# Kernel tuning notes

Hardware: AMD Instinct MI355X
Metric: run time of the kernel (lower is better)

The kernel has to match this reference:

```python
import jax, jax.numpy as jnp
import numpy as np
from itertools import product

N = 300000          # active voxels
CIN, C = 16, 32     # input / conv channels
K = 27              # 3x3x3 kernel volume
Z, Y, X = 41, 1024, 1024  # sparse spatial shape (grid_size[::-1] + [1,0,0])
B = 2               # batch size
EPS = 1e-3          # BatchNorm eps (matches norm_fn eps=0.001)


def _build_coords_and_rulebook(rng):
    # unique active coords per batch element
    total = Z * Y * X
    per = N // B
    coords = []
    for b in range(B):
        lin = np.unique(rng.integers(0, total, size=int(per * 1.3)))
        rng.shuffle(lin)
        lin = lin[:per]
        assert lin.shape[0] == per
        z = lin // (Y * X)
        y = (lin % (Y * X)) // X
        x = lin % X
        coords.append(np.stack([np.full(per, b), z, y, x], axis=1))
    coords = np.concatenate(coords, axis=0).astype(np.int64)  # [N,4]

    # hash-free rulebook via sorted linear keys + searchsorted
    key = ((coords[:, 0] * Z + coords[:, 1]) * Y + coords[:, 2]) * X + coords[:, 3]
    perm = np.argsort(key)
    skey = key[perm]
    nbr = np.full((N, K), -1, dtype=np.int32)
    bz, zz, yy, xx = coords[:, 0], coords[:, 1], coords[:, 2], coords[:, 3]
    for k, (dz, dy, dx) in enumerate(product((-1, 0, 1), repeat=3)):
        nz, ny, nx = zz + dz, yy + dy, xx + dx
        valid = (nz >= 0) & (nz < Z) & (ny >= 0) & (ny < Y) & (nx >= 0) & (nx < X)
        nkey = ((bz * Z + nz) * Y + ny) * X + nx
        pos = np.searchsorted(skey, nkey)
        pos = np.clip(pos, 0, N - 1)
        found = valid & (skey[pos] == nkey)
        nbr[:, k] = np.where(found, perm[pos], -1).astype(np.int32)
    return coords, nbr


def _bn_params(k, c):
    k1, k2, k3, k4 = jax.random.split(k, 4)
    gamma = jax.random.uniform(k1, (c,), minval=0.5, maxval=1.5)
    beta = jax.random.normal(k2, (c,)) * 0.1
    mean = jax.random.normal(k3, (c,)) * 0.1
    var = jax.random.uniform(k4, (c,), minval=0.5, maxval=1.5)
    return jnp.stack([gamma, beta, mean, var], axis=0)  # [4,C]


def setup_inputs() -> dict:
    rng = np.random.default_rng(0)
    _, nbr = _build_coords_and_rulebook(rng)

    key = jax.random.key(0)
    ks = jax.random.split(key, 12)
    feat = jax.random.normal(ks[0], (N, CIN), dtype=jnp.float32)

    def conv_w(k, cin, cout):
        return jax.random.normal(k, (K, cin, cout), dtype=jnp.float32) * (1.0 / np.sqrt(K * cin))

    return {
        "voxel_features": feat,
        "neighbor_idx": jnp.asarray(nbr),
        "w_in": conv_w(ks[1], CIN, C), "bn_in": _bn_params(ks[2], C),
        "w1a": conv_w(ks[3], C, C), "bn1a": _bn_params(ks[4], C),
        "w1b": conv_w(ks[5], C, C), "bn1b": _bn_params(ks[6], C),
        "w2a": conv_w(ks[7], C, C), "bn2a": _bn_params(ks[8], C),
        "w2b": conv_w(ks[9], C, C), "bn2b": _bn_params(ks[10], C),
    }


def reference(voxel_features, neighbor_idx, w_in, bn_in, w1a, bn1a, w1b, bn1b,
              w2a, bn2a, w2b, bn2b):
    def bn(x, p):
        gamma, beta, mean, var = p
        return gamma * (x - mean) * jax.lax.rsqrt(var + EPS) + beta

    def subm(feat, w):
        # submanifold conv: gather active neighbors, GEMM per kernel offset, accumulate
        out = jnp.zeros((feat.shape[0], w.shape[2]), feat.dtype)
        for k in range(K):
            idx = neighbor_idx[:, k]
            g = jnp.where((idx >= 0)[:, None], feat[jnp.maximum(idx, 0)], 0.0)
            out = out + g @ w[k]
        return out

    # conv_input: SubMConv3d + BN + ReLU
    x = jax.nn.relu(bn(subm(voxel_features, w_in), bn_in))
    # conv1: two SparseBasicBlocks (conv-bn-relu-conv-bn + residual, relu)
    for wa, bna, wb, bnb in ((w1a, bn1a, w1b, bn1b), (w2a, bn2a, w2b, bn2b)):
        identity = x
        x = jax.nn.relu(bn(subm(x, wa), bna))
        x = bn(subm(x, wb), bnb)
        x = jax.nn.relu(x + identity)
    # voxel importance (vis_importance branch, minus file IO / sorting side effects)
    voxel_importance = jax.nn.sigmoid(jnp.mean(jnp.abs(x), axis=1, keepdims=True))
    return x, voxel_importance
```

## Files before the change

### kernel.cpp

```cpp
#include <hip/hip_runtime.h>
#include <hip/hip_bf16.h>
#include <hip/hip_fp16.h>
#include <cstdint>
#include <cstddef>

#define NVOX 300000
#define KNBR 27
#define COUT 32
#define CINP 32
#define NT   (NVOX / 16)
#define RB   ((NVOX + 255) / 256)
#define WFIXE (5 * KNBR * CINP * COUT)
#define WFB  ((WFIXE + 255) / 256)
#define WDE  (5 * COUT * CINP)
#define WDB  ((WDE + 255) / 256)

typedef __hip_bfloat16 bf16;
typedef _Float16 half8 __attribute__((ext_vector_type(8)));
typedef float floatx4 __attribute__((ext_vector_type(4)));
typedef unsigned short ushort8 __attribute__((ext_vector_type(8)));

__device__ __forceinline__ float bf2f(unsigned short u) {
    union { unsigned int i; float f; } x; x.i = ((unsigned int)u) << 16; return x.f;
}
__device__ __forceinline__ int detect_fp32(const void* b0) {
    const unsigned short* p = (const unsigned short*)b0;
    int hits = 0;
    for (int i = 0; i < 16; i++) {
        float v = bf2f(p[2 * i]);
        if (v >= 0.25f && v <= 4.0f) hits++;
    }
    return (hits >= 8) ? 0 : 1;
}
__device__ __forceinline__ float rdw(const void* w, int rel, int fp32) {
    return fp32 ? ((const float*)w)[rel] : __bfloat162float(((const bf16*)w)[rel]);
}


__global__ __launch_bounds__(256)
void setup_kernel(const int* __restrict__ nbr,
                  const void* w0, const void* w1, const void* w2, const void* w3, const void* w4,
                  const void* b0, const void* b1, const void* b2, const void* b3, const void* b4,
                  float* __restrict__ wfix, __half* __restrict__ wtf,
                  float* __restrict__ bnab,
                  int* __restrict__ flag, int* __restrict__ counter,
                  int* __restrict__ cvlist) {
    const int tid = threadIdx.x;

    if (blockIdx.x < RB) {
        __shared__ int flags[256];
        __shared__ int wsum[4];
        __shared__ int wbase[4];
        flags[tid] = 0;
        __syncthreads();
        const int base = blockIdx.x * 256;
        const int nvox = (NVOX - base < 256) ? (NVOX - base) : 256;
        const int nI4  = (nvox * KNBR) >> 2;
        const int4* p4 = (const int4*)(nbr + (size_t)base * KNBR);
        for (int i = tid; i < nI4; i += 256) {
            const int4 q = p4[i];
            if ((q.x & q.y & q.z & q.w) < 0) continue;
            const unsigned t = (unsigned)(i << 2);
            if (q.x >= 0) { unsigned u = t;     unsigned lv = (u * 4855u) >> 17; if (u - lv * 27u != 13u) flags[lv] = 1; }
            if (q.y >= 0) { unsigned u = t + 1; unsigned lv = (u * 4855u) >> 17; if (u - lv * 27u != 13u) flags[lv] = 1; }
            if (q.z >= 0) { unsigned u = t + 2; unsigned lv = (u * 4855u) >> 17; if (u - lv * 27u != 13u) flags[lv] = 1; }
            if (q.w >= 0) { unsigned u = t + 3; unsigned lv = (u * 4855u) >> 17; if (u - lv * 27u != 13u) flags[lv] = 1; }
        }
        __syncthreads();
        const int v = base + tid;
        const bool f = (tid < nvox) && (flags[tid] != 0);
        const unsigned long long wm = __ballot(f);
        const int wd = tid >> 6, ln = tid & 63;
        if (ln == 0) wsum[wd] = __popcll(wm);
        __syncthreads();
        if (tid == 0) {
            int t0 = wsum[0], t1 = wsum[1], t2 = wsum[2], t3 = wsum[3];
            int tot = t0 + t1 + t2 + t3;
            int b = tot ? atomicAdd(counter, tot) : 0;
            wbase[0] = b; wbase[1] = b + t0; wbase[2] = b + t0 + t1; wbase[3] = b + t0 + t1 + t2;
        }
        __syncthreads();
        if (f) cvlist[wbase[wd] + __popcll(wm & ((1ULL << ln) - 1ULL))] = v;
        return;
    }

    const int fp32 = detect_fp32(b0);

    if (blockIdx.x < RB + WFB) {
        int i = (blockIdx.x - RB) * 256 + tid;
        if (i >= WFIXE) return;
        int L   = i / (KNBR * CINP * COUT);
        int rem = i % (KNBR * CINP * COUT);
        int k   = rem / (CINP * COUT);
        int kk  = (rem / COUT) % CINP;
        int nn  = rem % COUT;
        const void* w = (L == 0) ? w0 : (L == 1) ? w1 : (L == 2) ? w2 : (L == 3) ? w3 : w4;
        int cinL = (L == 0) ? 16 : 32;
        wfix[i] = (kk < cinL) ? rdw(w, (k * cinL + kk) * COUT + nn, fp32) : 0.f;
        return;
    }

    if (blockIdx.x < RB + WFB + WDB) {
        int i = (blockIdx.x - RB - WFB) * 256 + tid;
        if (i >= WDE) return;
        int L  = i / (COUT * CINP);
        int nn = (i / CINP) % COUT;
        int kk = i % CINP;
        const void* w = (L == 0) ? w0 : (L == 1) ? w1 : (L == 2) ? w2 : (L == 3) ? w3 : w4;
        int cinL = (L == 0) ? 16 : 32;
        int sk = (L == 0) ? kk : ((kk & 1) ? 16 + (kk >> 1) : (kk >> 1));
        float val = (sk < cinL) ? rdw(w, (13 * cinL + sk) * COUT + nn, fp32) : 0.f;
        wtf[i] = __float2half(val);
        return;
    }

    if (tid == 192) *flag = fp32;
    if (tid < 160) {
        int L = tid / 32, c = tid % 32;
        const void* b = (L == 0) ? b0 : (L == 1) ? b1 : (L == 2) ? b2 : (L == 3) ? b3 : b4;
        float g, be, m, v;
        if (fp32) {
            const float* q = (const float*)b;
            g = q[c]; be = q[32 + c]; m = q[64 + c]; v = q[96 + c];
        } else {
            const bf16* q = (const bf16*)b;
            g = __bfloat162float(q[c]); be = __bfloat162float(q[32 + c]);
            m = __bfloat162float(q[64 + c]); v = __bfloat162float(q[96 + c]);
        }
        float a = g * rsqrtf(v + 1e-3f);
        bnab[L * 64 + c]      = a;
        bnab[L * 64 + 32 + c] = be - a * m;
    }
}

__global__ __launch_bounds__(256)
void dense_fused(const void* __restrict__ feat,
                 const __half* __restrict__ wtf,
                 const float* __restrict__ bnab,
                 void* __restrict__ out_base,
                 const int* __restrict__ flag) {
    __shared__ __align__(16) _Float16 ldsT[4][16][40];
    const int gw   = (blockIdx.x * 256 + threadIdx.x) >> 6;
    const int nw   = (gridDim.x * 256) >> 6;
    const int wv   = threadIdx.x >> 6;
    const int lane = threadIdx.x & 63;
    const int n    = lane & 15;
    const int quad = lane >> 4;
    const int fp32 = *flag;

    half8 bfa[5], bfb[5];
    float a0[5], b0v[5], a1[5], b1v[5];
#pragma unroll
    for (int L = 0; L < 5; L++) {
        bfa[L] = *(const half8*)((const _Float16*)wtf + L * 1024 + n * 32 + quad * 8);
        bfb[L] = *(const half8*)((const _Float16*)wtf + L * 1024 + (n + 16) * 32 + quad * 8);
        a0[L] = bnab[L * 64 + n];      b0v[L] = bnab[L * 64 + 32 + n];
        a1[L] = bnab[L * 64 + 16 + n]; b1v[L] = bnab[L * 64 + 48 + n];
    }

    for (int t = gw; t < NT; t += nw) {
        const int v0 = t * 16;
        half8 af = {};
        if (quad < 2) {
            if (fp32) {
                const float* p = (const float*)feat + (size_t)(v0 + n) * 16 + quad * 8;
                const float4 u0 = *(const float4*)p;
                const float4 u1 = *(const float4*)(p + 4);
                af[0] = (_Float16)u0.x; af[1] = (_Float16)u0.y; af[2] = (_Float16)u0.z; af[3] = (_Float16)u0.w;
                af[4] = (_Float16)u1.x; af[5] = (_Float16)u1.y; af[6] = (_Float16)u1.z; af[7] = (_Float16)u1.w;
            } else {
                const ushort8 u = *(const ushort8*)((const unsigned short*)feat + (size_t)(v0 + n) * 16 + quad * 8);
#pragma unroll
                for (int j = 0; j < 8; j++) af[j] = (_Float16)bf2f(u[j]);
            }
        }
        float id0[4], id1[4];
#pragma unroll
        for (int L = 0; L < 5; L++) {
            floatx4 c0 = {0.f, 0.f, 0.f, 0.f}, c1 = {0.f, 0.f, 0.f, 0.f};
            c0 = __builtin_amdgcn_mfma_f32_16x16x32_f16(af, bfa[L], c0, 0, 0, 0);
            c1 = __builtin_amdgcn_mfma_f32_16x16x32_f16(af, bfb[L], c1, 0, 0, 0);
            if (L < 4) {
#pragma unroll
                for (int r = 0; r < 4; r++) {
                    float y0 = fmaf(a0[L], c0[r], b0v[L]);
                    float y1 = fmaf(a1[L], c1[r], b1v[L]);
                    if (L == 2) { y0 += id0[r]; y1 += id1[r]; }
                    y0 = fmaxf(y0, 0.f); y1 = fmaxf(y1, 0.f);
                    if (L == 0 || L == 2) { id0[r] = y0; id1[r] = y1; }
                    const int m = quad * 4 + r;
                    *reinterpret_cast<__half2*>(&ldsT[wv][m][2 * n]) = __floats2half2_rn(y0, y1);
                }
                af = *reinterpret_cast<const half8*>(&ldsT[wv][n][quad * 8]);
            } else {
#pragma unroll
                for (int r = 0; r < 4; r++) {
                    float y0 = fmaxf(fmaf(a0[4], c0[r], b0v[4]) + id0[r], 0.f);
                    float y1 = fmaxf(fmaf(a1[4], c1[r], b1v[4]) + id1[r], 0.f);
                    const int v = v0 + quad * 4 + r;
                    float s = y0 + y1;
#pragma unroll
                    for (int o = 1; o < 16; o <<= 1) s += __shfl_xor(s, o, 16);
                    const float imp = 1.0f / (1.0f + expf(-s * (1.0f / 32.0f)));
                    if (fp32) {
                        float* ox = (float*)out_base;
                        ox[(size_t)v * COUT + n]      = y0;
                        ox[(size_t)v * COUT + n + 16] = y1;
                        if (n == 0) ox[(size_t)NVOX * COUT + v] = imp;
                    } else {
                        bf16* ox = (bf16*)out_base;
                        ox[(size_t)v * COUT + n]      = __float2bfloat16(y0);
                        ox[(size_t)v * COUT + n + 16] = __float2bfloat16(y1);
                        if (n == 0) ox[(size_t)NVOX * COUT + v] = __float2bfloat16(imp);
                    }
                }
            }
        }
    }
}

template<bool IS_L0, bool HAS_RES, bool FINAL>
__global__ __launch_bounds__(256)
void fix_kernel(const void* __restrict__ inp,
                const int* __restrict__ nbr,
                const int* __restrict__ cvlist, const int* __restrict__ count,
                const float* __restrict__ wt,
                const float* __restrict__ bnab,
                const __half* __restrict__ res,
                __half* __restrict__ out,
                void* __restrict__ out_base,
                const int* __restrict__ flag) {
    const int gw   = (blockIdx.x * 256 + threadIdx.x) >> 6;
    const int nw   = (gridDim.x * 256) >> 6;
    const int lane = threadIdx.x & 63;
    const int c    = lane & 31;
    const int n    = *count;
    const int fp32io = *flag;

    for (int i = gw; i < n; i += nw) {
        const int v = cvlist[i];
        int idx = (lane < KNBR) ? nbr[(size_t)v * KNBR + lane] : -1;
        unsigned long long m = __ballot(idx >= 0) & ((1ULL << KNBR) - 1ULL);
        float acc0 = 0.f, acc1 = 0.f;
        while (m) {
            const int k0 = (int)__builtin_ctzll(m); m &= m - 1;
            int k1 = -1;
            if (m) { k1 = (int)__builtin_ctzll(m); m &= m - 1; }
            const int kme = (lane >= 32) ? k1 : k0;
            const bool act = (kme >= 0);
            const int kk = act ? kme : 0;
            const int src = __shfl(idx, kk, 64);
            float xv = 0.f;
            if (act) {
                if (IS_L0) {
                    if (c < 16)
                        xv = fp32io ? ((const float*)inp)[(size_t)src * 16 + c]
                                    : bf2f(((const unsigned short*)inp)[(size_t)src * 16 + c]);
                } else {
                    xv = __half2float(((const __half*)inp)[(size_t)src * CINP + c]);
                }
            }
            const float* wk = wt + (size_t)kk * (CINP * COUT) + c;
            const int JL = IS_L0 ? 16 : 32;
#pragma unroll
            for (int j = 0; j < 32; j += 2) {
                if (j >= JL) break;
                float xa = __shfl(xv, j, 32);
                float xb = __shfl(xv, j + 1, 32);
                acc0 = fmaf(xa, wk[j * COUT], acc0);
                acc1 = fmaf(xb, wk[(j + 1) * COUT], acc1);
            }
        }
        float acc = acc0 + acc1;
        acc += __shfl_xor(acc, 32, 64);
        float y = fmaf(bnab[c], acc, bnab[32 + c]);
        if (HAS_RES) y += __half2float(res[(size_t)v * COUT + c]);
        y = fmaxf(y, 0.f);

        if (FINAL) {
            float s2 = y;
#pragma unroll
            for (int o = 16; o > 0; o >>= 1) s2 += __shfl_xor(s2, o, 32);
            float imp = 1.0f / (1.0f + expf(-s2 * (1.0f / 32.0f)));
            if (fp32io) {
                float* ox = (float*)out_base;
                if (lane < 32) ox[(size_t)v * COUT + c] = y;
                if (lane == 0) ox[(size_t)NVOX * COUT + v] = imp;
            } else {
                bf16* ox = (bf16*)out_base;
                if (lane < 32) ox[(size_t)v * COUT + c] = __float2bfloat16(y);
                if (lane == 0) ox[(size_t)NVOX * COUT + v] = __float2bfloat16(imp);
            }
        } else {
            if (lane < 32) out[(size_t)v * COUT + c] = __float2half(y);
        }
    }
}

extern "C" void kernel_launch(void* const* d_in, const int* in_sizes, int n_in,
                              void* d_out, int out_size, void* d_ws, size_t ws_size,
                              hipStream_t stream) {
    char* ws = (char*)d_ws;
    int*    counter = (int*)ws;
    int*    flag    = counter + 1;
    int*    cvlist  = (int*)(ws + 256);
    float*  wfix    = (float*)((char*)cvlist + (size_t)NVOX * 4);
    float*  bnab    = wfix + WFIXE;
    __half* wtf     = (__half*)(bnab + 320);
    char*   after   = (char*)(wtf + WDE);
    __half* X0 = (__half*)((((uintptr_t)after) + 255) & ~(uintptr_t)255);
    __half* X1 = X0 + (size_t)NVOX * COUT;
    __half* X2 = X1 + (size_t)NVOX * COUT;

    const void* feat = d_in[0];
    const int*  nbr  = (const int*)d_in[1];

    hipMemsetAsync(counter, 0, 8, stream);

    setup_kernel<<<dim3(RB + WFB + WDB + 1), 256, 0, stream>>>(
        nbr, d_in[2], d_in[4], d_in[6], d_in[8], d_in[10],
        d_in[3], d_in[5], d_in[7], d_in[9], d_in[11],
        wfix, wtf, bnab, flag, counter, cvlist);

    dense_fused<<<dim3(1172), 256, 0, stream>>>(feat, wtf, bnab, d_out, flag);

    dim3 gf(2048);
    fix_kernel<true,  false, false><<<gf, 256, 0, stream>>>(feat, nbr, cvlist, counter, wfix + 0 * KNBR * CINP * COUT, bnab + 0 * 64, nullptr, X0, nullptr, flag);
    fix_kernel<false, false, false><<<gf, 256, 0, stream>>>(X0,   nbr, cvlist, counter, wfix + 1 * KNBR * CINP * COUT, bnab + 1 * 64, nullptr, X1, nullptr, flag);
    fix_kernel<false, true,  false><<<gf, 256, 0, stream>>>(X1,   nbr, cvlist, counter, wfix + 2 * KNBR * CINP * COUT, bnab + 2 * 64, X0,      X2, nullptr, flag);
    fix_kernel<false, false, false><<<gf, 256, 0, stream>>>(X2,   nbr, cvlist, counter, wfix + 3 * KNBR * CINP * COUT, bnab + 3 * 64, nullptr, X1, nullptr, flag);
    fix_kernel<false, true,  true ><<<gf, 256, 0, stream>>>(X1,   nbr, cvlist, counter, wfix + 4 * KNBR * CINP * COUT, bnab + 4 * 64, X2, nullptr, d_out, flag);
}
```

Before: 226.2 us.

## Fuse dense and fix stages into one cooperative persistent kernel with grid syncs

Replaces the dense kernel plus five fix-up kernel launches with a single cooperative kernel. It runs each fix layer, separates layers with grid-wide syncs, and splits the dense pass into four chunks that run alongside the fix layers. The aim is to cut launch and inter-kernel gap overhead and to use idle time in the small fix passes. It adds grid.sync costs and a grid capped at 1024 blocks, and falls back to the old launch sequence if the cooperative launch fails.

Result: slower. 704.6 us (+211.4%).

```diff
diff --git a/kernel.cpp b/kernel.cpp
--- a/kernel.cpp
+++ b/kernel.cpp
@@ -1,4 +1,5 @@
 #include <hip/hip_runtime.h>
+#include <hip/hip_cooperative_groups.h>
 #include <hip/hip_bf16.h>
 #include <hip/hip_fp16.h>
 #include <cstdint>
@@ -14,11 +15,14 @@
 #define WFB  ((WFIXE + 255) / 256)
 #define WDE  (5 * COUT * CINP)
 #define WDB  ((WDE + 255) / 256)
+#define WPL  (KNBR * CINP * COUT)
 
 typedef __hip_bfloat16 bf16;
 typedef _Float16 half8 __attribute__((ext_vector_type(8)));
 typedef float floatx4 __attribute__((ext_vector_type(4)));
 typedef unsigned short ushort8 __attribute__((ext_vector_type(8)));
+
+namespace cg = cooperative_groups;
 
 __device__ __forceinline__ float bf2f(unsigned short u) {
     union { unsigned int i; float f; } x; x.i = ((unsigned int)u) << 16; return x.f;
@@ -133,32 +137,27 @@
     }
 }
 
-__global__ __launch_bounds__(256)
-void dense_fused(const void* __restrict__ feat,
-                 const __half* __restrict__ wtf,
-                 const float* __restrict__ bnab,
-                 void* __restrict__ out_base,
-                 const int* __restrict__ flag) {
-    __shared__ __align__(16) _Float16 ldsT[4][16][40];
-    const int gw   = (blockIdx.x * 256 + threadIdx.x) >> 6;
-    const int nw   = (gridDim.x * 256) >> 6;
-    const int wv   = threadIdx.x >> 6;
-    const int lane = threadIdx.x & 63;
-    const int n    = lane & 15;
-    const int quad = lane >> 4;
-    const int fp32 = *flag;
-
-    half8 bfa[5], bfb[5];
-    float a0[5], b0v[5], a1[5], b1v[5];
+
+struct DW {
+    half8 wa[5], wb[5];
+    float ba[5], bb[5], bc[5], bd[5];
+};
+__device__ __forceinline__ void load_dw(DW& d, const __half* __restrict__ wtf,
+                                        const float* __restrict__ bnab, int n, int quad) {
 #pragma unroll
     for (int L = 0; L < 5; L++) {
-        bfa[L] = *(const half8*)((const _Float16*)wtf + L * 1024 + n * 32 + quad * 8);
-        bfb[L] = *(const half8*)((const _Float16*)wtf + L * 1024 + (n + 16) * 32 + quad * 8);
-        a0[L] = bnab[L * 64 + n];      b0v[L] = bnab[L * 64 + 32 + n];
-        a1[L] = bnab[L * 64 + 16 + n]; b1v[L] = bnab[L * 64 + 48 + n];
-    }
-
-    for (int t = gw; t < NT; t += nw) {
+        d.wa[L] = *(const half8*)((const _Float16*)wtf + L * 1024 + n * 32 + quad * 8);
+        d.wb[L] = *(const half8*)((const _Float16*)wtf + L * 1024 + (n + 16) * 32 + quad * 8);
+        d.ba[L] = bnab[L * 64 + n];      d.bb[L] = bnab[L * 64 + 32 + n];
+        d.bc[L] = bnab[L * 64 + 16 + n]; d.bd[L] = bnab[L * 64 + 48 + n];
+    }
+}
+
+__device__ __forceinline__ void dense_range(
+    int lo, int hi, int gw, int nw, const DW& dw,
+    const void* __restrict__ feat, int fp32, void* __restrict__ out_base,
+    _Float16 (* __restrict__ myT)[40], int n, int quad) {
+    for (int t = lo + gw; t < hi; t += nw) {
         const int v0 = t * 16;
         half8 af = {};
         if (quad < 2) {
@@ -178,25 +177,25 @@
 #pragma unroll
         for (int L = 0; L < 5; L++) {
             floatx4 c0 = {0.f, 0.f, 0.f, 0.f}, c1 = {0.f, 0.f, 0.f, 0.f};
-            c0 = __builtin_amdgcn_mfma_f32_16x16x32_f16(af, bfa[L], c0, 0, 0, 0);
-            c1 = __builtin_amdgcn_mfma_f32_16x16x32_f16(af, bfb[L], c1, 0, 0, 0);
+            c0 = __builtin_amdgcn_mfma_f32_16x16x32_f16(af, dw.wa[L], c0, 0, 0, 0);
+            c1 = __builtin_amdgcn_mfma_f32_16x16x32_f16(af, dw.wb[L], c1, 0, 0, 0);
             if (L < 4) {
 #pragma unroll
                 for (int r = 0; r < 4; r++) {
-                    float y0 = fmaf(a0[L], c0[r], b0v[L]);
-                    float y1 = fmaf(a1[L], c1[r], b1v[L]);
+                    float y0 = fmaf(dw.ba[L], c0[r], dw.bb[L]);
+                    float y1 = fmaf(dw.bc[L], c1[r], dw.bd[L]);
                     if (L == 2) { y0 += id0[r]; y1 += id1[r]; }
                     y0 = fmaxf(y0, 0.f); y1 = fmaxf(y1, 0.f);
                     if (L == 0 || L == 2) { id0[r] = y0; id1[r] = y1; }
                     const int m = quad * 4 + r;
-                    *reinterpret_cast<__half2*>(&ldsT[wv][m][2 * n]) = __floats2half2_rn(y0, y1);
+                    *reinterpret_cast<__half2*>(&myT[m][2 * n]) = __floats2half2_rn(y0, y1);
                 }
-                af = *reinterpret_cast<const half8*>(&ldsT[wv][n][quad * 8]);
+                af = *reinterpret_cast<const half8*>(&myT[n][quad * 8]);
             } else {
 #pragma unroll
                 for (int r = 0; r < 4; r++) {
-                    float y0 = fmaxf(fmaf(a0[4], c0[r], b0v[4]) + id0[r], 0.f);
-                    float y1 = fmaxf(fmaf(a1[4], c1[r], b1v[4]) + id1[r], 0.f);
+                    float y0 = fmaxf(fmaf(dw.ba[4], c0[r], dw.bb[4]) + id0[r], 0.f);
+                    float y1 = fmaxf(fmaf(dw.bc[4], c1[r], dw.bd[4]) + id1[r], 0.f);
                     const int v = v0 + quad * 4 + r;
                     float s = y0 + y1;
 #pragma unroll
@@ -219,25 +218,15 @@
     }
 }
 
-template<bool IS_L0, bool HAS_RES, bool FINAL>
-__global__ __launch_bounds__(256)
-void fix_kernel(const void* __restrict__ inp,
-                const int* __restrict__ nbr,
-                const int* __restrict__ cvlist, const int* __restrict__ count,
-                const float* __restrict__ wt,
-                const float* __restrict__ bnab,
-                const __half* __restrict__ res,
-                __half* __restrict__ out,
-                void* __restrict__ out_base,
-                const int* __restrict__ flag) {
-    const int gw   = (blockIdx.x * 256 + threadIdx.x) >> 6;
-    const int nw   = (gridDim.x * 256) >> 6;
-    const int lane = threadIdx.x & 63;
-    const int c    = lane & 31;
-    const int n    = *count;
-    const int fp32io = *flag;
-
-    for (int i = gw; i < n; i += nw) {
+template<int IS_L0, int HAS_RES, int FINAL>
+__device__ __forceinline__ void fix_range(
+    int nC, int gw, int nw, int lane,
+    const void* __restrict__ inp, const int* __restrict__ nbr,
+    const int* __restrict__ cvlist, const float* __restrict__ wt,
+    const float* __restrict__ bnab, const __half* __restrict__ res,
+    __half* __restrict__ out, void* __restrict__ out_base, int fp32io) {
+    const int c = lane & 31;
+    for (int i = gw; i < nC; i += nw) {
         const int v = cvlist[i];
         int idx = (lane < KNBR) ? nbr[(size_t)v * KNBR + lane] : -1;
         unsigned long long m = __ballot(idx >= 0) & ((1ULL << KNBR) - 1ULL);
@@ -297,6 +286,76 @@
     }
 }
 
+__global__ __launch_bounds__(256)
+void mega_kernel(const void* __restrict__ feat, const int* __restrict__ nbr,
+                 const int* __restrict__ cvlist, const int* __restrict__ counter,
+                 const float* __restrict__ wfix, const __half* __restrict__ wtf,
+                 const float* __restrict__ bnab,
+                 __half* __restrict__ X0, __half* __restrict__ X1, __half* __restrict__ X2,
+                 void* __restrict__ out_base, const int* __restrict__ flag) {
+    __shared__ __align__(16) _Float16 ldsT[4][16][40];
+    cg::grid_group grid = cg::this_grid();
+
+    const int gw   = (blockIdx.x * 256 + threadIdx.x) >> 6;
+    const int nw   = (gridDim.x * 256) >> 6;
+    const int wv   = threadIdx.x >> 6;
+    const int lane = threadIdx.x & 63;
+    const int n    = lane & 15;
+    const int quad = lane >> 4;
+    const int fp32 = *flag;
+    const int nC   = *counter;
+
+    DW dw; load_dw(dw, wtf, bnab, n, quad);
+
+    const int C1 = (NT * 1) / 4, C2 = (NT * 2) / 4, C3 = (NT * 3) / 4;
+
+    fix_range<1, 0, 0>(nC, gw, nw, lane, feat, nbr, cvlist, wfix + 0 * WPL, bnab + 0 * 64, nullptr, X0, nullptr, fp32);
+    dense_range(0, C1, gw, nw, dw, feat, fp32, out_base, ldsT[wv], n, quad);
+    __threadfence(); grid.sync(); __threadfence();
+
+    fix_range<0, 0, 0>(nC, gw, nw, lane, X0, nbr, cvlist, wfix + 1 * WPL, bnab + 1 * 64, nullptr, X1, nullptr, fp32);
+    dense_range(C1, C2, gw, nw, dw, feat, fp32, out_base, ldsT[wv], n, quad);
+    __threadfence(); grid.sync(); __threadfence();
+
+    fix_range<0, 1, 0>(nC, gw, nw, lane, X1, nbr, cvlist, wfix + 2 * WPL, bnab + 2 * 64, X0, X2, nullptr, fp32);
+    dense_range(C2, C3, gw, nw, dw, feat, fp32, out_base, ldsT[wv], n, quad);
+    __threadfence(); grid.sync(); __threadfence();
+
+    fix_range<0, 0, 0>(nC, gw, nw, lane, X2, nbr, cvlist, wfix + 3 * WPL, bnab + 3 * 64, nullptr, X1, nullptr, fp32);
+    dense_range(C3, NT, gw, nw, dw, feat, fp32, out_base, ldsT[wv], n, quad);
+    __threadfence(); grid.sync(); __threadfence();
+
+    fix_range<0, 1, 1>(nC, gw, nw, lane, X1, nbr, cvlist, wfix + 4 * WPL, bnab + 4 * 64, X2, nullptr, out_base, fp32);
+}
+
+__global__ __launch_bounds__(256)
+void dense_fused(const void* __restrict__ feat, const __half* __restrict__ wtf,
+                 const float* __restrict__ bnab, void* __restrict__ out_base,
+                 const int* __restrict__ flag) {
+    __shared__ __align__(16) _Float16 ldsT[4][16][40];
+    const int gw   = (blockIdx.x * 256 + threadIdx.x) >> 6;
+    const int nw   = (gridDim.x * 256) >> 6;
+    const int wv   = threadIdx.x >> 6;
+    const int lane = threadIdx.x & 63;
+    const int n    = lane & 15;
+    const int quad = lane >> 4;
+    DW dw; load_dw(dw, wtf, bnab, n, quad);
+    dense_range(0, NT, gw, nw, dw, feat, *flag, out_base, ldsT[wv], n, quad);
+}
+
+template<int IS_L0, int HAS_RES, int FINAL>
+__global__ __launch_bounds__(256)
+void fix_kernel(const void* __restrict__ inp, const int* __restrict__ nbr,
+                const int* __restrict__ cvlist, const int* __restrict__ count,
+                const float* __restrict__ wt, const float* __restrict__ bnab,
+                const __half* __restrict__ res, __half* __restrict__ out,
+                void* __restrict__ out_base, const int* __restrict__ flag) {
+    const int gw   = (blockIdx.x * 256 + threadIdx.x) >> 6;
+    const int nw   = (gridDim.x * 256) >> 6;
+    const int lane = threadIdx.x & 63;
+    fix_range<IS_L0, HAS_RES, FINAL>(*count, gw, nw, lane, inp, nbr, cvlist, wt, bnab, res, out, out_base, *flag);
+}
+
 extern "C" void kernel_launch(void* const* d_in, const int* in_sizes, int n_in,
                               void* d_out, int out_size, void* d_ws, size_t ws_size,
                               hipStream_t stream) {
@@ -322,12 +381,48 @@
         d_in[3], d_in[5], d_in[7], d_in[9], d_in[11],
         wfix, wtf, bnab, flag, counter, cvlist);
 
-    dense_fused<<<dim3(1172), 256, 0, stream>>>(feat, wtf, bnab, d_out, flag);
-
-    dim3 gf(2048);
-    fix_kernel<true,  false, false><<<gf, 256, 0, stream>>>(feat, nbr, cvlist, counter, wfix + 0 * KNBR * CINP * COUT, bnab + 0 * 64, nullptr, X0, nullptr, flag);
-    fix_kernel<false, false, false><<<gf, 256, 0, stream>>>(X0,   nbr, cvlist, counter, wfix + 1 * KNBR * CINP * COUT, bnab + 1 * 64, nullptr, X1, nullptr, flag);
-    fix_kernel<false, true,  false><<<gf, 256, 0, stream>>>(X1,   nbr, cvlist, counter, wfix + 2 * KNBR * CINP * COUT, bnab + 2 * 64, X0,      X2, nullptr, flag);
-    fix_kernel<false, false, false><<<gf, 256, 0, stream>>>(X2,   nbr, cvlist, counter, wfix + 3 * KNBR * CINP * COUT, bnab + 3 * 64, nullptr, X1, nullptr, flag);
-    fix_kernel<false, true,  true ><<<gf, 256, 0, stream>>>(X1,   nbr, cvlist, counter, wfix + 4 * KNBR * CINP * COUT, bnab + 4 * 64, X2, nullptr, d_out, flag);
-}
+    static int coop_grid = -2;
+    if (coop_grid == -2) {
+        int nb = 0;
+        if (hipOccupancyMaxActiveBlocksPerMultiprocessor(&nb, (const void*)mega_kernel, 256, 0) == hipSuccess && nb > 0) {
+            int ncu = 256;
+            hipDeviceProp_t prop;
+            if (hipGetDeviceProperties(&prop, 0) == hipSuccess && prop.multiProcessorCount > 0)
+                ncu = prop.multiProcessorCount;
+            long g = (long)nb * (long)ncu;
+            if (g > 1024) g = 1024;
+            if (g < 64)   g = 64;
+            coop_grid = (int)g;
+        } else {
+            coop_grid = -1;
+        }
+    }
+
+    bool launched = false;
+    if (coop_grid > 0) {
+        const int* cvl = cvlist; const int* cnt = counter;
+        const float* wfx = wfix; const __half* wtp = wtf; const float* bnp = bnab;
+        const int* flg = flag;
+        void* ka[12] = { (void*)&feat, (void*)&nbr, (void*)&cvl, (void*)&cnt,
+                         (void*)&wfx, (void*)&wtp, (void*)&bnp,
+                         (void*)&X0, (void*)&X1, (void*)&X2, (void*)&d_out, (void*)&flg };
+        hipError_t e = hipLaunchCooperativeKernel((const void*)mega_kernel,
+                                                  dim3(coop_grid), dim3(256), ka, 0, stream);
+        if (e == hipSuccess) {
+            launched = true;
+        } else {
+            (void)hipGetLastError();
+            coop_grid = -1;
+        }
+    }
+
+    if (!launched) {
+        dim3 gd(1172), gf(2048);
+        dense_fused<<<gd, 256, 0, stream>>>(feat, wtf, bnab, d_out, flag);
+        fix_kernel<1, 0, 0><<<gf, 256, 0, stream>>>(feat, nbr, cvlist, counter, wfix + 0 * WPL, bnab + 0 * 64, nullptr, X0, nullptr, flag);
+        fix_kernel<0, 0, 0><<<gf, 256, 0, stream>>>(X0,   nbr, cvlist, counter, wfix + 1 * WPL, bnab + 1 * 64, nullptr, X1, nullptr, flag);
+        fix_kernel<0, 1, 0><<<gf, 256, 0, stream>>>(X1,   nbr, cvlist, counter, wfix + 2 * WPL, bnab + 2 * 64, X0,      X2, nullptr, flag);
+        fix_kernel<0, 0, 0><<<gf, 256, 0, stream>>>(X2,   nbr, cvlist, counter, wfix + 3 * WPL, bnab + 3 * 64, nullptr, X1, nullptr, flag);
+        fix_kernel<0, 1, 1><<<gf, 256, 0, stream>>>(X1,   nbr, cvlist, counter, wfix + 4 * WPL, bnab + 4 * 64, X2, nullptr, d_out, flag);
+    }
+}
```

## Compact corrected voxels, precompute per-voxel tap lists, and fuse first fix into dense pass

Applied to the files above, without the earlier changes.

The setup pass now records each corrected voxel's compacted position. The first sparse-correction layer runs in the same launch as the dense center-tap pass. That layer also builds a per-voxel list of valid taps, each encoded as a compacted source index plus kernel offset. Later correction layers read this list instead of re-reading the neighbor table and re-balloting. They also keep intermediate features in compacted buffers, which shrinks their working set and improves locality. The cost is extra workspace for the tap lists and more work in the first correction pass.

New measurement: 221.9 us. Within noise of the previous version (-1.9%).

```diff
diff --git a/kernel.cpp b/kernel.cpp
--- a/kernel.cpp
+++ b/kernel.cpp
@@ -14,6 +14,9 @@
 #define WFB  ((WFIXE + 255) / 256)
 #define WDE  (5 * COUT * CINP)
 #define WDB  ((WDE + 255) / 256)
+#define WPL  (KNBR * CINP * COUT)
+#define GD   1172
+#define GF0  876
 
 typedef __hip_bfloat16 bf16;
 typedef _Float16 half8 __attribute__((ext_vector_type(8)));
@@ -44,7 +47,7 @@
                   float* __restrict__ wfix, __half* __restrict__ wtf,
                   float* __restrict__ bnab,
                   int* __restrict__ flag, int* __restrict__ counter,
-                  int* __restrict__ cvlist) {
+                  int* __restrict__ cvlist, int* __restrict__ corrpos) {
     const int tid = threadIdx.x;
 
     if (blockIdx.x < RB) {
@@ -80,7 +83,11 @@
             wbase[0] = b; wbase[1] = b + t0; wbase[2] = b + t0 + t1; wbase[3] = b + t0 + t1 + t2;
         }
         __syncthreads();
-        if (f) cvlist[wbase[wd] + __popcll(wm & ((1ULL << ln) - 1ULL))] = v;
+        if (f) {
+            int pos = wbase[wd] + __popcll(wm & ((1ULL << ln) - 1ULL));
+            cvlist[pos] = v;
+            corrpos[v]  = pos;
+        }
         return;
     }
 
@@ -133,31 +140,26 @@
     }
 }
 
-__global__ __launch_bounds__(256)
-void dense_fused(const void* __restrict__ feat,
-                 const __half* __restrict__ wtf,
-                 const float* __restrict__ bnab,
-                 void* __restrict__ out_base,
-                 const int* __restrict__ flag) {
-    __shared__ __align__(16) _Float16 ldsT[4][16][40];
-    const int gw   = (blockIdx.x * 256 + threadIdx.x) >> 6;
-    const int nw   = (gridDim.x * 256) >> 6;
-    const int wv   = threadIdx.x >> 6;
-    const int lane = threadIdx.x & 63;
-    const int n    = lane & 15;
-    const int quad = lane >> 4;
-    const int fp32 = *flag;
-
-    half8 bfa[5], bfb[5];
-    float a0[5], b0v[5], a1[5], b1v[5];
+
+struct DW {
+    half8 wa[5], wb[5];
+    float ba[5], bb[5], bc[5], bd[5];
+};
+__device__ __forceinline__ void load_dw(DW& d, const __half* __restrict__ wtf,
+                                        const float* __restrict__ bnab, int n, int quad) {
 #pragma unroll
     for (int L = 0; L < 5; L++) {
-        bfa[L] = *(const half8*)((const _Float16*)wtf + L * 1024 + n * 32 + quad * 8);
-        bfb[L] = *(const half8*)((const _Float16*)wtf + L * 1024 + (n + 16) * 32 + quad * 8);
-        a0[L] = bnab[L * 64 + n];      b0v[L] = bnab[L * 64 + 32 + n];
-        a1[L] = bnab[L * 64 + 16 + n]; b1v[L] = bnab[L * 64 + 48 + n];
-    }
-
+        d.wa[L] = *(const half8*)((const _Float16*)wtf + L * 1024 + n * 32 + quad * 8);
+        d.wb[L] = *(const half8*)((const _Float16*)wtf + L * 1024 + (n + 16) * 32 + quad * 8);
+        d.ba[L] = bnab[L * 64 + n];      d.bb[L] = bnab[L * 64 + 32 + n];
+        d.bc[L] = bnab[L * 64 + 16 + n]; d.bd[L] = bnab[L * 64 + 48 + n];
+    }
+}
+
+__device__ __forceinline__ void dense_range(
+    int gw, int nw, const DW& dw,
+    const void* __restrict__ feat, int fp32, void* __restrict__ out_base,
+    _Float16 (* __restrict__ myT)[40], int n, int quad) {
     for (int t = gw; t < NT; t += nw) {
         const int v0 = t * 16;
         half8 af = {};
@@ -178,25 +180,25 @@
 #pragma unroll
         for (int L = 0; L < 5; L++) {
             floatx4 c0 = {0.f, 0.f, 0.f, 0.f}, c1 = {0.f, 0.f, 0.f, 0.f};
-            c0 = __builtin_amdgcn_mfma_f32_16x16x32_f16(af, bfa[L], c0, 0, 0, 0);
-            c1 = __builtin_amdgcn_mfma_f32_16x16x32_f16(af, bfb[L], c1, 0, 0, 0);
+            c0 = __builtin_amdgcn_mfma_f32_16x16x32_f16(af, dw.wa[L], c0, 0, 0, 0);
+            c1 = __builtin_amdgcn_mfma_f32_16x16x32_f16(af, dw.wb[L], c1, 0, 0, 0);
             if (L < 4) {
 #pragma unroll
                 for (int r = 0; r < 4; r++) {
-                    float y0 = fmaf(a0[L], c0[r], b0v[L]);
-                    float y1 = fmaf(a1[L], c1[r], b1v[L]);
+                    float y0 = fmaf(dw.ba[L], c0[r], dw.bb[L]);
+                    float y1 = fmaf(dw.bc[L], c1[r], dw.bd[L]);
                     if (L == 2) { y0 += id0[r]; y1 += id1[r]; }
                     y0 = fmaxf(y0, 0.f); y1 = fmaxf(y1, 0.f);
                     if (L == 0 || L == 2) { id0[r] = y0; id1[r] = y1; }
                     const int m = quad * 4 + r;
-                    *reinterpret_cast<__half2*>(&ldsT[wv][m][2 * n]) = __floats2half2_rn(y0, y1);
+                    *reinterpret_cast<__half2*>(&myT[m][2 * n]) = __floats2half2_rn(y0, y1);
                 }
-                af = *reinterpret_cast<const half8*>(&ldsT[wv][n][quad * 8]);
+                af = *reinterpret_cast<const half8*>(&myT[n][quad * 8]);
             } else {
 #pragma unroll
                 for (int r = 0; r < 4; r++) {
-                    float y0 = fmaxf(fmaf(a0[4], c0[r], b0v[4]) + id0[r], 0.f);
-                    float y1 = fmaxf(fmaf(a1[4], c1[r], b1v[4]) + id1[r], 0.f);
+                    float y0 = fmaxf(fmaf(dw.ba[4], c0[r], dw.bb[4]) + id0[r], 0.f);
+                    float y1 = fmaxf(fmaf(dw.bc[4], c1[r], dw.bd[4]) + id1[r], 0.f);
                     const int v = v0 + quad * 4 + r;
                     float s = y0 + y1;
 #pragma unroll
@@ -219,28 +221,25 @@
     }
 }
 
-template<bool IS_L0, bool HAS_RES, bool FINAL>
-__global__ __launch_bounds__(256)
-void fix_kernel(const void* __restrict__ inp,
-                const int* __restrict__ nbr,
-                const int* __restrict__ cvlist, const int* __restrict__ count,
-                const float* __restrict__ wt,
-                const float* __restrict__ bnab,
-                const __half* __restrict__ res,
-                __half* __restrict__ out,
-                void* __restrict__ out_base,
-                const int* __restrict__ flag) {
-    const int gw   = (blockIdx.x * 256 + threadIdx.x) >> 6;
-    const int nw   = (gridDim.x * 256) >> 6;
-    const int lane = threadIdx.x & 63;
-    const int c    = lane & 31;
-    const int n    = *count;
-    const int fp32io = *flag;
-
-    for (int i = gw; i < n; i += nw) {
+__device__ __forceinline__ void fix0_range(
+    int nC, int gw, int nw, int lane,
+    const void* __restrict__ feat, const int* __restrict__ nbr,
+    const int* __restrict__ cvlist, const int* __restrict__ corrpos,
+    int* __restrict__ ctap,
+    const float* __restrict__ wt, const float* __restrict__ bnab,
+    __half* __restrict__ xout, int fp32) {
+    const int c = lane & 31;
+    for (int i = gw; i < nC; i += nw) {
         const int v = cvlist[i];
         int idx = (lane < KNBR) ? nbr[(size_t)v * KNBR + lane] : -1;
-        unsigned long long m = __ballot(idx >= 0) & ((1ULL << KNBR) - 1ULL);
+        const bool valid = idx >= 0;
+        unsigned long long m = __ballot(valid) & ((1ULL << KNBR) - 1ULL);
+        if (valid) {
+            int sp  = corrpos[idx];
+            int pos = __popcll(m & ((1ULL << lane) - 1ULL));
+            ctap[(size_t)i * 28 + 1 + pos] = (sp << 5) | lane;
+        }
+        if (lane == 0) ctap[(size_t)i * 28] = __popcll(m);
         float acc0 = 0.f, acc1 = 0.f;
         while (m) {
             const int k0 = (int)__builtin_ctzll(m); m &= m - 1;
@@ -251,20 +250,12 @@
             const int kk = act ? kme : 0;
             const int src = __shfl(idx, kk, 64);
             float xv = 0.f;
-            if (act) {
-                if (IS_L0) {
-                    if (c < 16)
-                        xv = fp32io ? ((const float*)inp)[(size_t)src * 16 + c]
-                                    : bf2f(((const unsigned short*)inp)[(size_t)src * 16 + c]);
-                } else {
-                    xv = __half2float(((const __half*)inp)[(size_t)src * CINP + c]);
-                }
-            }
+            if (act && c < 16)
+                xv = fp32 ? ((const float*)feat)[(size_t)src * 16 + c]
+                          : bf2f(((const unsigned short*)feat)[(size_t)src * 16 + c]);
             const float* wk = wt + (size_t)kk * (CINP * COUT) + c;
-            const int JL = IS_L0 ? 16 : 32;
-#pragma unroll
-            for (int j = 0; j < 32; j += 2) {
-                if (j >= JL) break;
+#pragma unroll
+            for (int j = 0; j < 16; j += 2) {
                 float xa = __shfl(xv, j, 32);
                 float xb = __shfl(xv, j + 1, 32);
                 acc0 = fmaf(xa, wk[j * COUT], acc0);
@@ -273,8 +264,45 @@
         }
         float acc = acc0 + acc1;
         acc += __shfl_xor(acc, 32, 64);
+        float y = fmaxf(fmaf(bnab[c], acc, bnab[32 + c]), 0.f);
+        if (lane < 32) xout[(size_t)i * COUT + c] = __float2half(y);
+    }
+}
+
+template<int HAS_RES, int FINAL>
+__device__ __forceinline__ void fixc_range(
+    int nC, int gw, int nw, int lane,
+    const __half* __restrict__ xin, const int* __restrict__ ctap,
+    const int* __restrict__ cvlist,
+    const float* __restrict__ wt, const float* __restrict__ bnab,
+    const __half* __restrict__ res,
+    __half* __restrict__ xout, void* __restrict__ out_base, int fp32io) {
+    const int c = lane & 31;
+    for (int i = gw; i < nC; i += nw) {
+        const size_t tb = (size_t)i * 28;
+        const int cnt = ctap[tb];
+        const int tp  = (lane < cnt) ? ctap[tb + 1 + lane] : 0;
+        float acc0 = 0.f, acc1 = 0.f;
+        for (int t = 0; t < cnt; t += 2) {
+            const bool actB = (t + 1) < cnt;
+            const int sel = (lane >= 32 && actB) ? (t + 1) : t;
+            const int tap = __shfl(tp, sel, 64);
+            const bool act = (lane < 32) || actB;
+            const int sp = tap >> 5, kk = tap & 31;
+            const float xv = act ? __half2float(xin[(size_t)sp * COUT + c]) : 0.f;
+            const float* wk = wt + (size_t)kk * (CINP * COUT) + c;
+#pragma unroll
+            for (int j = 0; j < 32; j += 2) {
+                float xa = __shfl(xv, j, 32);
+                float xb = __shfl(xv, j + 1, 32);
+                acc0 = fmaf(xa, wk[j * COUT], acc0);
+                acc1 = fmaf(xb, wk[(j + 1) * COUT], acc1);
+            }
+        }
+        float acc = acc0 + acc1;
+        acc += __shfl_xor(acc, 32, 64);
         float y = fmaf(bnab[c], acc, bnab[32 + c]);
-        if (HAS_RES) y += __half2float(res[(size_t)v * COUT + c]);
+        if (HAS_RES) y += __half2float(res[(size_t)i * COUT + c]);
         y = fmaxf(y, 0.f);
 
         if (FINAL) {
@@ -282,6 +310,7 @@
 #pragma unroll
             for (int o = 16; o > 0; o >>= 1) s2 += __shfl_xor(s2, o, 32);
             float imp = 1.0f / (1.0f + expf(-s2 * (1.0f / 32.0f)));
+            const int v = cvlist[i];
             if (fp32io) {
                 float* ox = (float*)out_base;
                 if (lane < 32) ox[(size_t)v * COUT + c] = y;
@@ -292,9 +321,50 @@
                 if (lane == 0) ox[(size_t)NVOX * COUT + v] = __float2bfloat16(imp);
             }
         } else {
-            if (lane < 32) out[(size_t)v * COUT + c] = __float2half(y);
-        }
-    }
+            if (lane < 32) xout[(size_t)i * COUT + c] = __float2half(y);
+        }
+    }
+}
+
+
+__global__ __launch_bounds__(256)
+void phase0_kernel(const void* __restrict__ feat, const int* __restrict__ nbr,
+                   const int* __restrict__ cvlist, const int* __restrict__ corrpos,
+                   const int* __restrict__ counter, int* __restrict__ ctap,
+                   const float* __restrict__ wfix, const __half* __restrict__ wtf,
+                   const float* __restrict__ bnab,
+                   __half* __restrict__ Xc0, void* __restrict__ out_base,
+                   const int* __restrict__ flag) {
+    __shared__ __align__(16) _Float16 ldsT[4][16][40];
+    const int lane = threadIdx.x & 63;
+    const int fp32 = *flag;
+    if (blockIdx.x < GD) {
+        const int gw = (blockIdx.x * 256 + threadIdx.x) >> 6;
+        const int nw = (GD * 256) >> 6;
+        const int wv = threadIdx.x >> 6;
+        const int n = lane & 15, quad = lane >> 4;
+        DW dw; load_dw(dw, wtf, bnab, n, quad);
+        dense_range(gw, nw, dw, feat, fp32, out_base, ldsT[wv], n, quad);
+    } else {
+        const int gw = ((blockIdx.x - GD) * 256 + threadIdx.x) >> 6;
+        const int nw = (GF0 * 256) >> 6;
+        fix0_range(*counter, gw, nw, lane, feat, nbr, cvlist, corrpos, ctap,
+                   wfix, bnab, Xc0, fp32);
+    }
+}
+
+template<int HAS_RES, int FINAL>
+__global__ __launch_bounds__(256)
+void fixc_kernel(const __half* __restrict__ xin, const int* __restrict__ ctap,
+                 const int* __restrict__ cvlist, const int* __restrict__ count,
+                 const float* __restrict__ wt, const float* __restrict__ bnab,
+                 const __half* __restrict__ res, __half* __restrict__ xout,
+                 void* __restrict__ out_base, const int* __restrict__ flag) {
+    const int gw   = (blockIdx.x * 256 + threadIdx.x) >> 6;
+    const int nw   = (gridDim.x * 256) >> 6;
+    const int lane = threadIdx.x & 63;
+    fixc_range<HAS_RES, FINAL>(*count, gw, nw, lane, xin, ctap, cvlist, wt, bnab,
+                               res, xout, out_base, *flag);
 }
 
 extern "C" void kernel_launch(void* const* d_in, const int* in_sizes, int n_in,
@@ -304,13 +374,15 @@
     int*    counter = (int*)ws;
     int*    flag    = counter + 1;
     int*    cvlist  = (int*)(ws + 256);
-    float*  wfix    = (float*)((char*)cvlist + (size_t)NVOX * 4);
+    int*    corrpos = cvlist + NVOX;
+    int*    ctap    = corrpos + NVOX;
+    float*  wfix    = (float*)(ctap + (size_t)NVOX * 28);
     float*  bnab    = wfix + WFIXE;
     __half* wtf     = (__half*)(bnab + 320);
     char*   after   = (char*)(wtf + WDE);
-    __half* X0 = (__half*)((((uintptr_t)after) + 255) & ~(uintptr_t)255);
-    __half* X1 = X0 + (size_t)NVOX * COUT;
-    __half* X2 = X1 + (size_t)NVOX * COUT;
+    __half* Xc0 = (__half*)((((uintptr_t)after) + 255) & ~(uintptr_t)255);
+    __half* Xc1 = Xc0 + (size_t)NVOX * COUT;
+    __half* Xc2 = Xc1 + (size_t)NVOX * COUT;
 
     const void* feat = d_in[0];
     const int*  nbr  = (const int*)d_in[1];
@@ -320,14 +392,14 @@
     setup_kernel<<<dim3(RB + WFB + WDB + 1), 256, 0, stream>>>(
         nbr, d_in[2], d_in[4], d_in[6], d_in[8], d_in[10],
         d_in[3], d_in[5], d_in[7], d_in[9], d_in[11],
-        wfix, wtf, bnab, flag, counter, cvlist);
-
-    dense_fused<<<dim3(1172), 256, 0, stream>>>(feat, wtf, bnab, d_out, flag);
+        wfix, wtf, bnab, flag, counter, cvlist, corrpos);
+
+    phase0_kernel<<<dim3(GD + GF0), 256, 0, stream>>>(
+        feat, nbr, cvlist, corrpos, counter, ctap, wfix, wtf, bnab, Xc0, d_out, flag);
 
     dim3 gf(2048);
-    fix_kernel<true,  false, false><<<gf, 256, 0, stream>>>(feat, nbr, cvlist, counter, wfix + 0 * KNBR * CINP * COUT, bnab + 0 * 64, nullptr, X0, nullptr, flag);
-    fix_kernel<false, false, false><<<gf, 256, 0, stream>>>(X0,   nbr, cvlist, counter, wfix + 1 * KNBR * CINP * COUT, bnab + 1 * 64, nullptr, X1, nullptr, flag);
-    fix_kernel<false, true,  false><<<gf, 256, 0, stream>>>(X1,   nbr, cvlist, counter, wfix + 2 * KNBR * CINP * COUT, bnab + 2 * 64, X0,      X2, nullptr, flag);
-    fix_kernel<false, false, false><<<gf, 256, 0, stream>>>(X2,   nbr, cvlist, counter, wfix + 3 * KNBR * CINP * COUT, bnab + 3 * 64, nullptr, X1, nullptr, flag);
-    fix_kernel<false, true,  true ><<<gf, 256, 0, stream>>>(X1,   nbr, cvlist, counter, wfix + 4 * KNBR * CINP * COUT, bnab + 4 * 64, X2, nullptr, d_out, flag);
-}
+    fixc_kernel<0, 0><<<gf, 256, 0, stream>>>(Xc0, ctap, cvlist, counter, wfix + 1 * WPL, bnab + 1 * 64, nullptr, Xc1, nullptr, flag);
+    fixc_kernel<1, 0><<<gf, 256, 0, stream>>>(Xc1, ctap, cvlist, counter, wfix + 2 * WPL, bnab + 2 * 64, Xc0,     Xc2, nullptr, flag);
+    fixc_kernel<0, 0><<<gf, 256, 0, stream>>>(Xc2, ctap, cvlist, counter, wfix + 3 * WPL, bnab + 3 * 64, nullptr, Xc1, nullptr, flag);
+    fixc_kernel<1, 1><<<gf, 256, 0, stream>>>(Xc1, ctap, cvlist, counter, wfix + 4 * WPL, bnab + 4 * 64, Xc2, nullptr, d_out, flag);
+}
```
